# Performance work log

Hardware: AMD Instinct MI355X
Metric: run time of the kernel (lower is better)

The kernel has to match this reference:

```python
import jax, jax.numpy as jnp
import numpy as np

C = 128
B = 64
EPS = 1e-6


def _ln2d(x, w, b):
    # LayerNorm over channel dim (NAFNet-style LayerNorm2d), eps=1e-6
    mu = x.mean(axis=1, keepdims=True)
    var = ((x - mu) ** 2).mean(axis=1, keepdims=True)
    return (x - mu) / jnp.sqrt(var + EPS) * w[None, :, None, None] + b[None, :, None, None]


def _conv4(x, w, b):
    # Conv2d kernel 4, stride 4, no padding; NCHW / OIHW
    y = jax.lax.conv_general_dilated(x, w, (4, 4), 'VALID',
                                     dimension_numbers=('NCHW', 'OIHW', 'NCHW'))
    return y + b[None, :, None, None]


def _pixel_shuffle4(x):
    # (B, c*16, H, W) -> (B, c, 4H, 4W), torch PixelShuffle semantics
    b, c16, h, w = x.shape
    c = c16 // 16
    x = x.reshape(b, c, 4, 4, h, w)
    x = x.transpose(0, 1, 4, 2, 5, 3)
    return x.reshape(b, c, h * 4, w * 4)


def setup_inputs() -> dict:
    key = jax.random.key(0)
    ks = jax.random.split(key, 16)
    s = 0.02
    return {
        'x_l': jax.random.normal(ks[0], (B, C, 32, 32), jnp.float32),
        'x_r': jax.random.normal(ks[1], (B, C, 32, 32), jnp.float32),
        'ln_w_l': jnp.ones((C,), jnp.float32), 'ln_b_l': jnp.zeros((C,), jnp.float32),
        'ln_w_r': jnp.ones((C,), jnp.float32), 'ln_b_r': jnp.zeros((C,), jnp.float32),
        'Wl1': jax.random.normal(ks[2], (C, C, 4, 4), jnp.float32) * s,
        'bl1': jnp.zeros((C,), jnp.float32),
        'Wr1': jax.random.normal(ks[3], (C, C, 4, 4), jnp.float32) * s,
        'br1': jnp.zeros((C,), jnp.float32),
        'Wl2': jax.random.normal(ks[4], (C, C, 4, 4), jnp.float32) * s,
        'bl2': jnp.zeros((C,), jnp.float32),
        'Wr2': jax.random.normal(ks[5], (C, C, 4, 4), jnp.float32) * s,
        'br2': jnp.zeros((C,), jnp.float32),
        'pos': jax.random.normal(ks[6], (1, C, 8, 8), jnp.float32),
        'beta': jax.random.normal(ks[7], (1, C, 1, 1), jnp.float32) * s,
        'gamma': jax.random.normal(ks[8], (1, C, 1, 1), jnp.float32) * s,
        'Wl3': jax.random.normal(ks[9], (16 * C, C), jnp.float32) * s,
        'bl3': jnp.zeros((16 * C,), jnp.float32),
        'Wr3': jax.random.normal(ks[10], (16 * C, C), jnp.float32) * s,
        'br3': jnp.zeros((16 * C,), jnp.float32),
    }


def reference(x_l, x_r, ln_w_l, ln_b_l, ln_w_r, ln_b_r, Wl1, bl1, Wr1, br1,
              Wl2, bl2, Wr2, br2, pos, beta, gamma, Wl3, bl3, Wr3, br3):
    c = x_l.shape[1]
    scale = c ** (-0.5)
    B1 = x_l.shape[0]
    B2 = x_r.shape[0]

    Ql = _conv4(_ln2d(x_l, ln_w_l, ln_b_l), Wl1, bl1) + pos  # (B1,c,8,8)
    Qr = _conv4(_ln2d(x_r, ln_w_r, ln_b_r), Wr1, br1) + pos  # (B2,c,8,8)
    h1, w1 = Ql.shape[-2], Ql.shape[-1]
    h2, w2 = Qr.shape[-2], Qr.shape[-1]
    m1, m2 = h1 * w1, h2 * w2

    Qlm = Ql.transpose(0, 2, 3, 1).reshape(B1, m1, c)          # b (h w) c
    Qrm = Qr.transpose(1, 0, 2, 3).reshape(c, B2 * m2)         # c (b h w)
    Vl = (_conv4(x_l, Wl2, bl2) + pos).transpose(0, 2, 3, 1).reshape(B1 * m1, c)
    Vr = (_conv4(x_r, Wr2, br2) + pos).transpose(0, 2, 3, 1).reshape(B2 * m2, c)

    attn = jnp.matmul(Qlm, Qrm) * scale                        # (B1, m1, B2*m2)

    F_r2l = jnp.matmul(jax.nn.softmax(attn * (B2 ** (-0.5)), axis=-1), Vr)
    F_r2l = F_r2l.reshape(B1, h1, w1, c)

    attn2 = attn.reshape(B1, m1, B2, m2).transpose(2, 3, 0, 1).reshape(B2, m2, B1 * m1)
    F_l2r = jnp.matmul(jax.nn.softmax(attn2 * (B1 ** (-0.5)), axis=-1), Vl)
    F_l2r = F_l2r.reshape(B2, h2, w2, c)

    F_r2l = _pixel_shuffle4((jnp.matmul(F_r2l, Wl3.T) + bl3).transpose(0, 3, 1, 2)) * beta
    F_l2r = _pixel_shuffle4((jnp.matmul(F_l2r, Wr3.T) + br3).transpose(0, 3, 1, 2)) * gamma
    return (x_l + F_r2l, x_r + F_l2r)
```

## Files before the change

kernel.cpp:

```cpp
#include <hip/hip_runtime.h>
#include <stdint.h>

using bf16x8 = __attribute__((ext_vector_type(8))) short;
using f32x4  = __attribute__((ext_vector_type(4))) float;

__device__ __forceinline__ unsigned short f2bf(float f) {
  union { float f; uint32_t u; } v; v.f = f;
  uint32_t r = v.u + 0x7FFFu + ((v.u >> 16) & 1u);
  return (unsigned short)(r >> 16);
}
__device__ __forceinline__ uint32_t pk2(float a, float b) {
  return (uint32_t)f2bf(a) | ((uint32_t)f2bf(b) << 16);
}
__device__ __forceinline__ float bf2f(unsigned short s) {
  union { uint32_t u; float f; } v; v.u = ((uint32_t)s) << 16;
  return v.f;
}
__device__ __forceinline__ f32x4 mfma16(bf16x8 a, bf16x8 b, f32x4 c) {
  return __builtin_amdgcn_mfma_f32_16x16x32_bf16(a, b, c, 0, 0, 0);
}

__global__ __launch_bounds__(256) void k_prep(
    const float* __restrict__ xl, const float* __restrict__ xr,
    const float* __restrict__ lnwl, const float* __restrict__ lnbl,
    const float* __restrict__ lnwr, const float* __restrict__ lnbr,
    const float* __restrict__ Wl1, const float* __restrict__ bl1,
    const float* __restrict__ Wr1, const float* __restrict__ br1,
    const float* __restrict__ Wl2, const float* __restrict__ Wr2,
    const float* __restrict__ Wl3, const float* __restrict__ Wr3,
    float* __restrict__ muW, float* __restrict__ rsW,
    unsigned short* __restrict__ Wq, unsigned short* __restrict__ Wv,
    float* __restrict__ bqW, unsigned short* __restrict__ W3bf)
{
  const int gbid = blockIdx.x;
  const int t = threadIdx.x;
  __shared__ float red[4];

  if (gbid < 256) {
    const int bx = gbid;
    const int side = bx >> 7, rem = bx & 127;
    const int b = rem >> 1, half = rem & 1;
    const float* x = (side ? xr : xl) + (size_t)b * 131072 + half * 512;
    const int px = t * 2;
    float s0=0, s1=0, q0=0, q1=0;
#pragma unroll 4
    for (int c = 0; c < 128; ++c) {
      const float2 v = *(const float2*)(x + c*1024 + px);
      s0 += v.x; q0 += v.x*v.x;
      s1 += v.y; q1 += v.y*v.y;
    }
    const int o = (side*64 + b)*1024 + half*512 + px;
    float2 mu, rs;
    mu.x = s0*(1.0f/128.0f); mu.y = s1*(1.0f/128.0f);
    rs.x = rsqrtf(fmaxf(q0*(1.0f/128.0f) - mu.x*mu.x, 0.0f) + 1e-6f);
    rs.y = rsqrtf(fmaxf(q1*(1.0f/128.0f) - mu.y*mu.y, 0.0f) + 1e-6f);
    *(float2*)(muW + o) = mu;
    *(float2*)(rsW + o) = rs;
  } else if (gbid < 512) {
    const int bx = gbid - 256;
    const int side = bx >> 7, co = bx & 127;
    const float* W1  = side ? Wr1 : Wl1;
    const float* W2  = side ? Wr2 : Wl2;
    const float* b1  = side ? br1 : bl1;
    const float* lnw = side ? lnwr : lnwl;
    const float* lnb = side ? lnbr : lnbl;
    const int ci = t >> 1;
    const float lw = lnw[ci], lb = lnb[ci];

    const size_t dsto = (size_t)(side*32 + (t>>3))*8192 + (size_t)co*64 + (t&7)*8;

    const float* src1 = W1 + (size_t)co*2048 + t*8;
    const float4 a0 = *(const float4*)(src1);
    const float4 a1 = *(const float4*)(src1 + 4);
    float part = (a0.x+a0.y+a0.z+a0.w + a1.x+a1.y+a1.z+a1.w) * lb;
    uint4 pkq;
    pkq.x = pk2(a0.x*lw, a0.y*lw); pkq.y = pk2(a0.z*lw, a0.w*lw);
    pkq.z = pk2(a1.x*lw, a1.y*lw); pkq.w = pk2(a1.z*lw, a1.w*lw);
    *(uint4*)(Wq + dsto) = pkq;

    const float* src2 = W2 + (size_t)co*2048 + t*8;
    const float4 c0 = *(const float4*)(src2);
    const float4 c1 = *(const float4*)(src2 + 4);
    uint4 pkv;
    pkv.x = pk2(c0.x, c0.y); pkv.y = pk2(c0.z, c0.w);
    pkv.z = pk2(c1.x, c1.y); pkv.w = pk2(c1.z, c1.w);
    *(uint4*)(Wv + dsto) = pkv;

    float v = part;
    v += __shfl_down(v, 32, 64); v += __shfl_down(v, 16, 64);
    v += __shfl_down(v, 8, 64);  v += __shfl_down(v, 4, 64);
    v += __shfl_down(v, 2, 64);  v += __shfl_down(v, 1, 64);
    if ((t & 63) == 0) red[t >> 6] = v;
    __syncthreads();
    if (t == 0) bqW[side*128 + co] = b1[co] + red[0] + red[1] + red[2] + red[3];
  } else {
    const int b = gbid - 512;
    const float* src = (b < 256 ? Wl3 : Wr3) + (size_t)(b & 255) * 1024;
    const float4 v = *(const float4*)(src + t*4);
    *(uint2*)(W3bf + (size_t)b*1024 + t*4) = make_uint2(pk2(v.x, v.y), pk2(v.z, v.w));
  }
}

__global__ __launch_bounds__(256) void k_conv(
    const float* __restrict__ xl, const float* __restrict__ xr,
    const unsigned short* __restrict__ Wq, const unsigned short* __restrict__ Wv,
    const float* __restrict__ muW, const float* __restrict__ rsW,
    unsigned short* __restrict__ Cpart)
{
  const int bid = blockIdx.x;
  const int ks = bid & 3;
  const int img = (bid >> 2) & 63;
  const int ctype = bid >> 8;
  const int side = ctype & 1;
  const bool isQ = ctype < 2;
  const float* x = (side ? xr : xl) + (size_t)img * 131072;
  const unsigned short* Bsrc = (isQ ? Wq : Wv) + (size_t)side * 262144;

  const int t = threadIdx.x;
  const int w = t >> 6, l = t & 63, lo = l & 15, g = l >> 4;

  __shared__ __align__(16) unsigned char lds[24576];
  unsigned char* A = lds;
  unsigned char* B = lds + 8192;

  const int cl   = t >> 6;
  const int px0  = (t & 63) * 16;
  const int y    = px0 >> 5;
  const int wr   = y & 3;
  const int pbase = (y >> 2)*8 + ((px0 & 31) >> 2);

  float4 mu4[4], rs4[4];
  if (isQ) {
    const int o = (side*64 + img)*1024 + px0;
#pragma unroll
    for (int i = 0; i < 4; ++i) {
      mu4[i] = *(const float4*)(muW + o + 4*i);
      rs4[i] = *(const float4*)(rsW + o + 4*i);
    }
  }

  const int cout = t >> 1, part = t & 1;
  const int keyB = ((cout ^ (cout >> 3)) & 7) << 4;

  f32x4 acc[4][2];
#pragma unroll
  for (int a = 0; a < 4; ++a) { acc[a][0] = (f32x4)0.0f; acc[a][1] = (f32x4)0.0f; }

  for (int it = 0; it < 8; ++it) {
    const int kb = ks*8 + it;
    __syncthreads();
    {
      const float* xs = x + (size_t)(kb*4 + cl)*1024 + px0;
#pragma unroll
      for (int i = 0; i < 4; ++i) {
        float4 v = *(const float4*)(xs + 4*i);
        if (isQ) {
          v.x = (v.x - mu4[i].x)*rs4[i].x; v.y = (v.y - mu4[i].y)*rs4[i].y;
          v.z = (v.z - mu4[i].z)*rs4[i].z; v.w = (v.w - mu4[i].w)*rs4[i].w;
        }
        const int p = pbase + i;
        int dst = p*128 + cl*32 + wr*8;
        dst ^= ((p ^ (p >> 3)) & 7) << 4;
        *(uint2*)(A + dst) = make_uint2(pk2(v.x, v.y), pk2(v.z, v.w));
      }
    }
    {
      const unsigned short* bs = Bsrc + (size_t)kb*8192 + t*32;
#pragma unroll
      for (int i = 0; i < 4; ++i) {
        const bf16x8 v = *(const bf16x8*)(bs + i*8);
        *(bf16x8*)(B + cout*128 + ((part*64 + i*16) ^ keyB)) = v;
      }
    }
    __syncthreads();
    bf16x8 af[4][2], bfr[2][2];
#pragma unroll
    for (int mf = 0; mf < 4; ++mf) {
      const int row = mf*16 + lo;
      const int key = ((row ^ (row >> 3)) & 7) << 4;
#pragma unroll
      for (int kc = 0; kc < 2; ++kc)
        af[mf][kc] = *(const bf16x8*)(A + row*128 + ((kc*64 + g*16) ^ key));
    }
#pragma unroll
    for (int nf = 0; nf < 2; ++nf) {
      const int row = w*32 + nf*16 + lo;
      const int key = ((row ^ (row >> 3)) & 7) << 4;
#pragma unroll
      for (int kc = 0; kc < 2; ++kc)
        bfr[nf][kc] = *(const bf16x8*)(B + row*128 + ((kc*64 + g*16) ^ key));
    }
    __builtin_amdgcn_s_setprio(1);
#pragma unroll
    for (int kc = 0; kc < 2; ++kc)
#pragma unroll
      for (int nf = 0; nf < 2; ++nf)
#pragma unroll
        for (int mf = 0; mf < 4; ++mf)
          acc[mf][nf] = mfma16(af[mf][kc], bfr[nf][kc], acc[mf][nf]);
    __builtin_amdgcn_s_setprio(0);
  }

  unsigned short* Cp = Cpart + (size_t)bid * 8192;
#pragma unroll
  for (int mf = 0; mf < 4; ++mf)
#pragma unroll
    for (int nf = 0; nf < 2; ++nf) {
      const int c = w*32 + nf*16 + lo;
      const int p0 = mf*16 + g*4;
      *(uint2*)(Cp + c*64 + p0) =
          make_uint2(pk2(acc[mf][nf][0], acc[mf][nf][1]),
                     pk2(acc[mf][nf][2], acc[mf][nf][3]));
    }
}

__global__ __launch_bounds__(256) void k_convred(
    const unsigned short* __restrict__ Cpart,
    const float* __restrict__ bqW,
    const float* __restrict__ bl2, const float* __restrict__ br2,
    const float* __restrict__ pos,
    unsigned short* __restrict__ Qbf, unsigned short* __restrict__ Vtbf)
{
  const int bid2 = blockIdx.x;
  const int ctype = bid2 >> 6, img = bid2 & 63;
  const int side = ctype & 1;
  const bool isQ = ctype < 2;
  const int t = threadIdx.x;

  __shared__ float S[64][130];

  const int c = t >> 1, p0 = (t & 1) * 32;
  {
    float acc[32];
#pragma unroll
    for (int j = 0; j < 32; ++j) acc[j] = 0.f;
#pragma unroll
    for (int s = 0; s < 4; ++s) {
      const unsigned short* Cp = Cpart + ((size_t)(bid2*4 + s))*8192 + c*64 + p0;
#pragma unroll
      for (int j8 = 0; j8 < 4; ++j8) {
        const bf16x8 v = *(const bf16x8*)(Cp + j8*8);
#pragma unroll
        for (int e = 0; e < 8; ++e)
          acc[j8*8 + e] += bf2f((unsigned short)v[e]);
      }
    }
#pragma unroll
    for (int j = 0; j < 32; ++j) S[p0 + j][c] = acc[j];
  }
  __syncthreads();

  if (isQ) {
    const float* bq = bqW + side*128;
    const int p = t >> 2, c0 = (t & 3) * 32;
    const int rot = (t & 3) * 4;
    uint32_t pk[16];
#pragma unroll
    for (int j2 = 0; j2 < 16; ++j2) {
      const int jj = (j2 + rot) & 15;
      const int ca = c0 + jj*2;
      const float2 sv = *(const float2*)(&S[p][ca]);
      const float va = (sv.x + bq[ca]     + pos[ca*64 + p])     * 0.12625283f;
      const float vb = (sv.y + bq[ca + 1] + pos[(ca+1)*64 + p]) * 0.12625283f;
      pk[jj] = pk2(va, vb);
    }
    unsigned short* Qo = Qbf + (size_t)side*524288 + ((size_t)(img*64 + p))*128 + c0;
    *(uint4*)(Qo)      = make_uint4(pk[0],  pk[1],  pk[2],  pk[3]);
    *(uint4*)(Qo + 8)  = make_uint4(pk[4],  pk[5],  pk[6],  pk[7]);
    *(uint4*)(Qo + 16) = make_uint4(pk[8],  pk[9],  pk[10], pk[11]);
    *(uint4*)(Qo + 24) = make_uint4(pk[12], pk[13], pk[14], pk[15]);
  } else {
    const float* b2 = side ? br2 : bl2;
    const float bb = b2[c];
    uint32_t pk[16];
#pragma unroll
    for (int j2 = 0; j2 < 16; ++j2) {
      const int pa = p0 + j2*2;
      const float va = S[pa][c]     + bb + pos[c*64 + pa];
      const float vb = S[pa + 1][c] + bb + pos[c*64 + pa + 1];
      pk[j2] = pk2(va, vb);
    }
    unsigned short* Vo = Vtbf + (size_t)side*524288 + (size_t)c*4096 + img*64 + p0;
    *(uint4*)(Vo)      = make_uint4(pk[0],  pk[1],  pk[2],  pk[3]);
    *(uint4*)(Vo + 8)  = make_uint4(pk[4],  pk[5],  pk[6],  pk[7]);
    *(uint4*)(Vo + 16) = make_uint4(pk[8],  pk[9],  pk[10], pk[11]);
    *(uint4*)(Vo + 24) = make_uint4(pk[12], pk[13], pk[14], pk[15]);
  }
}

__global__ __launch_bounds__(256, 2) void k_attn(
    const unsigned short* __restrict__ Qbf,
    const unsigned short* __restrict__ Vtbf,
    float* __restrict__ Opart,
    float* __restrict__ Lpart)
{
  const int bid = blockIdx.x;
  const int xcd = bid & 7;
  const int dir = xcd >> 2;
  const int ks  = xcd & 3;
  const int qb  = bid >> 3;
  const unsigned short* Qp = Qbf  + (size_t)dir*524288;
  const unsigned short* Kp = Qbf  + (size_t)(1-dir)*524288;
  const unsigned short* Vp = Vtbf + (size_t)(1-dir)*524288;

  const int t = threadIdx.x;
  const int w = t >> 6, l = t & 63, lo = l & 15, g = l >> 4;

  __shared__ __align__(16) unsigned char lds[73728];
  unsigned char* ldsP = lds + 65536;
  __shared__ float lred[4][64];

  bf16x8 aq[4][4];
#pragma unroll
  for (int mf = 0; mf < 4; ++mf)
#pragma unroll
    for (int kc = 0; kc < 4; ++kc)
      aq[mf][kc] = *(const bf16x8*)(Qp + (size_t)(qb*64 + mf*16 + lo)*128 + kc*32 + g*8);

  f32x4 o[4][2];
#pragma unroll
  for (int a = 0; a < 4; ++a) { o[a][0] = (f32x4)0.0f; o[a][1] = (f32x4)0.0f; }
  float ls[4] = {0.f, 0.f, 0.f, 0.f};

  const int kt0 = ks * 16;

  const int ksrcBase = t ^ ((t >> 4) & 7);
  const int vc    = t >> 3;
  const int vi16  = (t & 7) * 16;
  const int vsoff = (vi16 ^ (((t >> 3) & 7) << 4)) >> 1;

  {
    const uint4* src = (const uint4*)(Kp + (size_t)kt0*8192);
#pragma unroll
    for (int j = 0; j < 4; ++j)
      *(uint4*)(lds + (t + 256*j)*16) = src[ksrcBase + 256*j];
#pragma unroll
    for (int j = 0; j < 4; ++j) {
      const int c = vc + 32*j;
      *(uint4*)(lds + 32768 + c*128 + vi16) =
          *(const uint4*)(Vp + (size_t)c*4096 + kt0*64 + vsoff);
    }
  }
  __syncthreads();

  for (int it = 0; it < 16; ++it) {
    const int cur = it & 1;
    unsigned char* curK = lds + cur*16384;
    unsigned char* curV = lds + 32768 + cur*16384;

    uint4 kr0, kr1, kr2, kr3, vr0, vr1, vr2, vr3;
    if (it < 15) {
      const int kt = kt0 + it + 1;
      const uint4* src = (const uint4*)(Kp + (size_t)kt*8192);
      kr0 = src[ksrcBase];
      kr1 = src[ksrcBase + 256];
      kr2 = src[ksrcBase + 512];
      kr3 = src[ksrcBase + 768];
      const unsigned short* vsrc = Vp + (size_t)kt*64 + vsoff;
      vr0 = *(const uint4*)(vsrc + (size_t)(vc     )*4096);
      vr1 = *(const uint4*)(vsrc + (size_t)(vc + 32)*4096);
      vr2 = *(const uint4*)(vsrc + (size_t)(vc + 64)*4096);
      vr3 = *(const uint4*)(vsrc + (size_t)(vc + 96)*4096);
    }

    f32x4 s[4];
    s[0] = (f32x4)0.0f; s[1] = (f32x4)0.0f; s[2] = (f32x4)0.0f; s[3] = (f32x4)0.0f;
    const int krow = w*16 + lo;
    const int keyk = (krow & 7) << 4;
    __builtin_amdgcn_s_setprio(1);
#pragma unroll
    for (int kc = 0; kc < 4; ++kc) {
      const bf16x8 bk = *(const bf16x8*)(curK + krow*256 + ((kc*64 + g*16) ^ keyk));
#pragma unroll
      for (int mf = 0; mf < 4; ++mf)
        s[mf] = mfma16(bk, aq[mf][kc], s[mf]);
    }
    __builtin_amdgcn_s_setprio(0);

#pragma unroll
    for (int mf = 0; mf < 4; ++mf) {
      const float e0 = exp2f(s[mf][0]);
      const float e1 = exp2f(s[mf][1]);
      const float e2 = exp2f(s[mf][2]);
      const float e3 = exp2f(s[mf][3]);
      ls[mf] += (e0 + e1) + (e2 + e3);
      const int q = mf*16 + lo;
      const int koff = (w*32 + g*8) ^ ((q & 7) << 4);
      *(uint2*)(ldsP + q*128 + koff) = make_uint2(pk2(e0, e1), pk2(e2, e3));
    }
    __syncthreads();

    __builtin_amdgcn_s_setprio(1);
#pragma unroll
    for (int kd = 0; kd < 2; ++kd) {
      bf16x8 pa[4];
#pragma unroll
      for (int mf = 0; mf < 4; ++mf) {
        const int q = mf*16 + lo;
        pa[mf] = *(const bf16x8*)(ldsP + q*128 + ((kd*64 + g*16) ^ ((q & 7) << 4)));
      }
#pragma unroll
      for (int nf = 0; nf < 2; ++nf) {
        const int c = w*32 + nf*16 + lo;
        const bf16x8 bv = *(const bf16x8*)(curV + c*128 + ((kd*64 + g*16) ^ ((c & 7) << 4)));
#pragma unroll
        for (int mf = 0; mf < 4; ++mf)
          o[mf][nf] = mfma16(pa[mf], bv, o[mf][nf]);
      }
    }
    __builtin_amdgcn_s_setprio(0);

    if (it < 15) {
      unsigned char* nK = lds + (cur ^ 1)*16384;
      unsigned char* nV = lds + 32768 + (cur ^ 1)*16384;
      *(uint4*)(nK + (t      )*16) = kr0;
      *(uint4*)(nK + (t + 256)*16) = kr1;
      *(uint4*)(nK + (t + 512)*16) = kr2;
      *(uint4*)(nK + (t + 768)*16) = kr3;
      *(uint4*)(nV + (vc     )*128 + vi16) = vr0;
      *(uint4*)(nV + (vc + 32)*128 + vi16) = vr1;
      *(uint4*)(nV + (vc + 64)*128 + vi16) = vr2;
      *(uint4*)(nV + (vc + 96)*128 + vi16) = vr3;
    }
    __syncthreads();
  }

#pragma unroll
  for (int mf = 0; mf < 4; ++mf) {
    float v = ls[mf];
    v += __shfl_xor(v, 16, 64);
    v += __shfl_xor(v, 32, 64);
    if (l < 16) lred[w][mf*16 + lo] = v;
  }
  __syncthreads();

  float* Ob = Opart + (((size_t)dir*64 + qb)*4 + ks)*64*128;
#pragma unroll
  for (int mf = 0; mf < 4; ++mf)
#pragma unroll
    for (int nf = 0; nf < 2; ++nf) {
      const int c = w*32 + nf*16 + lo;
#pragma unroll
      for (int rr = 0; rr < 4; ++rr) {
        const int q = mf*16 + g*4 + rr;
        Ob[q*128 + c] = o[mf][nf][rr];
      }
    }
  if (t < 64)
    Lpart[(((size_t)dir*64 + qb)*4 + ks)*64 + t] =
        lred[0][t] + lred[1][t] + lred[2][t] + lred[3][t];
}

__global__ __launch_bounds__(256) void k_reduce(
    const float* __restrict__ Opart, const float* __restrict__ Lpart,
    unsigned short* __restrict__ Fbf)
{
  const int bid = blockIdx.x;
  const int dir = bid >> 7, rb = bid & 127;
  const int t = threadIdx.x;
  const int qr = t >> 3;
  const int cs = (t & 7) * 16;
  const int r  = rb*32 + qr;
  const int qb = r >> 6, q = r & 63;
  const size_t pb = ((size_t)dir*64 + qb)*4;
  float acc[16];
#pragma unroll
  for (int i = 0; i < 16; ++i) acc[i] = 0.f;
  float lsum = 0.f;
#pragma unroll
  for (int s = 0; s < 4; ++s) {
    const float* Ob = Opart + ((pb + s)*64 + q)*128 + cs;
#pragma unroll
    for (int i = 0; i < 16; i += 4) {
      const float4 v = *(const float4*)(Ob + i);
      acc[i] += v.x; acc[i+1] += v.y; acc[i+2] += v.z; acc[i+3] += v.w;
    }
    lsum += Lpart[(pb + s)*64 + q];
  }
  const float inv = 1.0f / lsum;
  uint32_t pkw[8];
#pragma unroll
  for (int i = 0; i < 8; ++i) pkw[i] = pk2(acc[2*i]*inv, acc[2*i+1]*inv);
  unsigned short* Fo = Fbf + (size_t)dir*524288 + (size_t)r*128 + cs;
  *(uint4*)(Fo)     = make_uint4(pkw[0], pkw[1], pkw[2], pkw[3]);
  *(uint4*)(Fo + 8) = make_uint4(pkw[4], pkw[5], pkw[6], pkw[7]);
}

__global__ __launch_bounds__(256) void k_proj(
    const unsigned short* __restrict__ Fbf,
    const unsigned short* __restrict__ W3bf,
    const float* __restrict__ bl3, const float* __restrict__ br3,
    const float* __restrict__ beta, const float* __restrict__ gamma,
    const float* __restrict__ xl, const float* __restrict__ xr,
    float* __restrict__ out)
{
  const int nb = blockIdx.x, mb = blockIdx.y, side = blockIdx.z;
  const unsigned short* F  = Fbf + (size_t)side*524288 + (size_t)mb*8192;
  const unsigned short* W3 = W3bf + (size_t)side*262144 + (size_t)nb*16384;
  const float* b3  = (side ? br3 : bl3) + nb*128;
  const float* scl = side ? gamma : beta;
  const float* xin = (side ? xr : xl) + (size_t)mb*131072;
  float* op = out + (size_t)side*8388608 + (size_t)mb*131072;

  const int t = threadIdx.x;
  const int w = t >> 6, l = t & 63, lo = l & 15, g = l >> 4;

  __shared__ __align__(16) unsigned char lds[49152];
  unsigned char* Ft = lds;
  unsigned char* B3 = lds + 16384;
  float* Sf = (float*)lds;

  {
    const uint4* src = (const uint4*)F;
#pragma unroll
    for (int j = 0; j < 4; ++j) {
      const int idx = t + 256*j;
      const int dst = idx*16;
      const int row = dst >> 8;
      *(uint4*)(Ft + dst) = src[(dst ^ ((row & 7) << 4)) >> 4];
    }
  }
  {
    const int nl = t >> 1, half = t & 1;
    const unsigned short* wsrc = W3 + (size_t)nl*128 + half*64;
#pragma unroll
    for (int ch = 0; ch < 8; ++ch) {
      const uint4 v = *(const uint4*)(wsrc + ch*8);
      const int inrow = (half*128 + ch*16) ^ ((nl & 7) << 4);
      *(uint4*)(B3 + nl*256 + inrow) = v;
    }
  }
  __syncthreads();

  f32x4 acc[4][2];
#pragma unroll
  for (int a=0;a<4;a++) { acc[a][0] = (f32x4)0.0f; acc[a][1] = (f32x4)0.0f; }

  bf16x8 af[4][4];
#pragma unroll
  for (int mf = 0; mf < 4; ++mf) {
    const int row = mf*16 + lo;
#pragma unroll
    for (int kc = 0; kc < 4; ++kc)
      af[mf][kc] = *(const bf16x8*)(Ft + row*256 + ((kc*64 + g*16) ^ ((row & 7) << 4)));
  }
#pragma unroll
  for (int kc = 0; kc < 4; ++kc)
#pragma unroll
    for (int nf = 0; nf < 2; ++nf) {
      const int n = w*32 + nf*16 + lo;
      const bf16x8 bb = *(const bf16x8*)(B3 + n*256 + ((kc*64 + g*16) ^ ((n & 7) << 4)));
#pragma unroll
      for (int mf = 0; mf < 4; ++mf)
        acc[mf][nf] = mfma16(af[mf][kc], bb, acc[mf][nf]);
    }

  __syncthreads();

  {
    const int r4 = (lo >> 2) & 3, sc = lo & 3;
#pragma unroll
    for (int nf = 0; nf < 2; ++nf) {
      const int cl = w*2 + nf;
      const int n16 = w*32 + nf*16 + lo;
      const float scc = scl[nb*8 + cl];
      const float bb3 = b3[n16];
#pragma unroll
      for (int mf = 0; mf < 4; ++mf)
#pragma unroll
        for (int rr = 0; rr < 4; ++rr) {
          const int pi = mf*16 + g*4 + rr;
          const int h = pi >> 3, wc = pi & 7;
          Sf[cl*1032 + h*128 + r4*32 + wc*4 + sc] = scc*(acc[mf][nf][rr] + bb3);
        }
    }
  }
  __syncthreads();

#pragma unroll
  for (int j = 0; j < 8; ++j) {
    const int pix = t*4;
    const float4 s = *(const float4*)(Sf + j*1032 + pix);
    const size_t gaddr = (size_t)(nb*8 + j)*1024 + pix;
    const float4 xv = *(const float4*)(xin + gaddr);
    float4 r;
    r.x = xv.x + s.x; r.y = xv.y + s.y; r.z = xv.z + s.z; r.w = xv.w + s.w;
    *(float4*)(op + gaddr) = r;
  }
}

extern "C" void kernel_launch(void* const* d_in, const int* in_sizes, int n_in,
                              void* d_out, int out_size, void* d_ws, size_t ws_size,
                              hipStream_t stream) {
  (void)in_sizes; (void)n_in; (void)out_size; (void)ws_size;
  const float* xl   = (const float*)d_in[0];
  const float* xr   = (const float*)d_in[1];
  const float* lnwl = (const float*)d_in[2];
  const float* lnbl = (const float*)d_in[3];
  const float* lnwr = (const float*)d_in[4];
  const float* lnbr = (const float*)d_in[5];
  const float* Wl1  = (const float*)d_in[6];
  const float* bl1  = (const float*)d_in[7];
  const float* Wr1  = (const float*)d_in[8];
  const float* br1  = (const float*)d_in[9];
  const float* Wl2  = (const float*)d_in[10];
  const float* bl2  = (const float*)d_in[11];
  const float* Wr2  = (const float*)d_in[12];
  const float* br2  = (const float*)d_in[13];
  const float* pos  = (const float*)d_in[14];
  const float* beta = (const float*)d_in[15];
  const float* gamma= (const float*)d_in[16];
  const float* Wl3  = (const float*)d_in[17];
  const float* bl3  = (const float*)d_in[18];
  const float* Wr3  = (const float*)d_in[19];
  const float* br3  = (const float*)d_in[20];

  float* muW = (float*)d_ws;
  float* rsW = muW + 131072;
  float* bqW = rsW + 131072;
  unsigned short* Wq   = (unsigned short*)(bqW + 256);
  unsigned short* Wv   = Wq + 524288;
  unsigned short* Qbf  = Wv + 524288;
  unsigned short* Vtbf = Qbf + 1048576;
  unsigned short* Fbf  = Vtbf + 1048576;
  unsigned short* W3bf = Fbf + 1048576;
  unsigned short* Cpart = W3bf + 524288;
  float* Opart = (float*)Cpart;
  float* Lpart = (float*)(Cpart + 8388608);

  k_prep<<<1024, 256, 0, stream>>>(xl, xr, lnwl, lnbl, lnwr, lnbr,
      Wl1, bl1, Wr1, br1, Wl2, Wr2, Wl3, Wr3, muW, rsW, Wq, Wv, bqW, W3bf);
  k_conv<<<1024, 256, 0, stream>>>(xl, xr, Wq, Wv, muW, rsW, Cpart);
  k_convred<<<256, 256, 0, stream>>>(Cpart, bqW, bl2, br2, pos, Qbf, Vtbf);
  k_attn<<<512, 256, 0, stream>>>(Qbf, Vtbf, Opart, Lpart);
  k_reduce<<<256, 256, 0, stream>>>(Opart, Lpart, Fbf);
  k_proj<<<dim3(16, 64, 2), 256, 0, stream>>>(Fbf, W3bf, bl3, br3,
      beta, gamma, xl, xr, (float*)d_out);
}
```

Measured before the change: 123.1 us.

## Split attention key range eight ways with single-buffered LDS for higher occupancy

The attention kernel now splits the key dimension into 8 chunks instead of 4, which doubles the grid to 1024 blocks, and the reduce kernel sums 8 partials. LDS drops from double-buffered K/V (about 73 KB) to a single buffer (40 KB), and the launch bound is raised to 4 blocks per CU, aiming for more waves in flight and better latency hiding. The costs are an extra barrier per iteration, since the next tile's writes must wait for all reads, and twice as much partial O/L traffic written and then read by the reduce kernel. The block-to-XCD mapping also changes: all 8 splits of a query block now share one block-id group instead of being spread by XCD.

After: 176.4 us. 43.3% more time.

```diff
diff --git a/kernel.cpp b/kernel.cpp
--- a/kernel.cpp
+++ b/kernel.cpp
@@ -288,17 +288,16 @@
   }
 }
 
-__global__ __launch_bounds__(256, 2) void k_attn(
+__global__ __launch_bounds__(256, 4) void k_attn(
     const unsigned short* __restrict__ Qbf,
     const unsigned short* __restrict__ Vtbf,
     float* __restrict__ Opart,
     float* __restrict__ Lpart)
 {
   const int bid = blockIdx.x;
-  const int xcd = bid & 7;
-  const int dir = xcd >> 2;
-  const int ks  = xcd & 3;
-  const int qb  = bid >> 3;
+  const int ks  = bid & 7;
+  const int dir = (bid >> 3) & 1;
+  const int qb  = bid >> 4;
   const unsigned short* Qp = Qbf  + (size_t)dir*524288;
   const unsigned short* Kp = Qbf  + (size_t)(1-dir)*524288;
   const unsigned short* Vp = Vtbf + (size_t)(1-dir)*524288;
@@ -306,9 +305,11 @@
   const int t = threadIdx.x;
   const int w = t >> 6, l = t & 63, lo = l & 15, g = l >> 4;
 
-  __shared__ __align__(16) unsigned char lds[73728];
-  unsigned char* ldsP = lds + 65536;
-  __shared__ float lred[4][64];
+  __shared__ __align__(16) unsigned char lds[40960];
+  unsigned char* Kb = lds;
+  unsigned char* Vb = lds + 16384;
+  unsigned char* Pb = lds + 32768;
+  float* lred = (float*)lds;
 
   bf16x8 aq[4][4];
 #pragma unroll
@@ -322,7 +323,7 @@
   for (int a = 0; a < 4; ++a) { o[a][0] = (f32x4)0.0f; o[a][1] = (f32x4)0.0f; }
   float ls[4] = {0.f, 0.f, 0.f, 0.f};
 
-  const int kt0 = ks * 16;
+  const int kt0 = ks * 8;
 
   const int ksrcBase = t ^ ((t >> 4) & 7);
   const int vc    = t >> 3;
@@ -333,23 +334,19 @@
     const uint4* src = (const uint4*)(Kp + (size_t)kt0*8192);
 #pragma unroll
     for (int j = 0; j < 4; ++j)
-      *(uint4*)(lds + (t + 256*j)*16) = src[ksrcBase + 256*j];
+      *(uint4*)(Kb + (t + 256*j)*16) = src[ksrcBase + 256*j];
 #pragma unroll
     for (int j = 0; j < 4; ++j) {
       const int c = vc + 32*j;
-      *(uint4*)(lds + 32768 + c*128 + vi16) =
+      *(uint4*)(Vb + c*128 + vi16) =
           *(const uint4*)(Vp + (size_t)c*4096 + kt0*64 + vsoff);
     }
   }
   __syncthreads();
 
-  for (int it = 0; it < 16; ++it) {
-    const int cur = it & 1;
-    unsigned char* curK = lds + cur*16384;
-    unsigned char* curV = lds + 32768 + cur*16384;
-
+  for (int it = 0; it < 8; ++it) {
     uint4 kr0, kr1, kr2, kr3, vr0, vr1, vr2, vr3;
-    if (it < 15) {
+    if (it < 7) {
       const int kt = kt0 + it + 1;
       const uint4* src = (const uint4*)(Kp + (size_t)kt*8192);
       kr0 = src[ksrcBase];
@@ -370,7 +367,7 @@
     __builtin_amdgcn_s_setprio(1);
 #pragma unroll
     for (int kc = 0; kc < 4; ++kc) {
-      const bf16x8 bk = *(const bf16x8*)(curK + krow*256 + ((kc*64 + g*16) ^ keyk));
+      const bf16x8 bk = *(const bf16x8*)(Kb + krow*256 + ((kc*64 + g*16) ^ keyk));
 #pragma unroll
       for (int mf = 0; mf < 4; ++mf)
         s[mf] = mfma16(bk, aq[mf][kc], s[mf]);
@@ -386,7 +383,7 @@
       ls[mf] += (e0 + e1) + (e2 + e3);
       const int q = mf*16 + lo;
       const int koff = (w*32 + g*8) ^ ((q & 7) << 4);
-      *(uint2*)(ldsP + q*128 + koff) = make_uint2(pk2(e0, e1), pk2(e2, e3));
+      *(uint2*)(Pb + q*128 + koff) = make_uint2(pk2(e0, e1), pk2(e2, e3));
     }
     __syncthreads();
 
@@ -397,32 +394,31 @@
 #pragma unroll
       for (int mf = 0; mf < 4; ++mf) {
         const int q = mf*16 + lo;
-        pa[mf] = *(const bf16x8*)(ldsP + q*128 + ((kd*64 + g*16) ^ ((q & 7) << 4)));
+        pa[mf] = *(const bf16x8*)(Pb + q*128 + ((kd*64 + g*16) ^ ((q & 7) << 4)));
       }
 #pragma unroll
       for (int nf = 0; nf < 2; ++nf) {
         const int c = w*32 + nf*16 + lo;
-        const bf16x8 bv = *(const bf16x8*)(curV + c*128 + ((kd*64 + g*16) ^ ((c & 7) << 4)));
+        const bf16x8 bv = *(const bf16x8*)(Vb + c*128 + ((kd*64 + g*16) ^ ((c & 7) << 4)));
 #pragma unroll
         for (int mf = 0; mf < 4; ++mf)
           o[mf][nf] = mfma16(pa[mf], bv, o[mf][nf]);
       }
     }
     __builtin_amdgcn_s_setprio(0);
-
-    if (it < 15) {
-      unsigned char* nK = lds + (cur ^ 1)*16384;
-      unsigned char* nV = lds + 32768 + (cur ^ 1)*16384;
-      *(uint4*)(nK + (t      )*16) = kr0;
-      *(uint4*)(nK + (t + 256)*16) = kr1;
-      *(uint4*)(nK + (t + 512)*16) = kr2;
-      *(uint4*)(nK + (t + 768)*16) = kr3;
-      *(uint4*)(nV + (vc     )*128 + vi16) = vr0;
-      *(uint4*)(nV + (vc + 32)*128 + vi16) = vr1;
-      *(uint4*)(nV + (vc + 64)*128 + vi16) = vr2;
-      *(uint4*)(nV + (vc + 96)*128 + vi16) = vr3;
-    }
     __syncthreads();
+
+    if (it < 7) {
+      *(uint4*)(Kb + (t      )*16) = kr0;
+      *(uint4*)(Kb + (t + 256)*16) = kr1;
+      *(uint4*)(Kb + (t + 512)*16) = kr2;
+      *(uint4*)(Kb + (t + 768)*16) = kr3;
+      *(uint4*)(Vb + (vc     )*128 + vi16) = vr0;
+      *(uint4*)(Vb + (vc + 32)*128 + vi16) = vr1;
+      *(uint4*)(Vb + (vc + 64)*128 + vi16) = vr2;
+      *(uint4*)(Vb + (vc + 96)*128 + vi16) = vr3;
+      __syncthreads();
+    }
   }
 
 #pragma unroll
@@ -430,11 +426,11 @@
     float v = ls[mf];
     v += __shfl_xor(v, 16, 64);
     v += __shfl_xor(v, 32, 64);
-    if (l < 16) lred[w][mf*16 + lo] = v;
+    if (l < 16) lred[w*64 + mf*16 + lo] = v;
   }
   __syncthreads();
 
-  float* Ob = Opart + (((size_t)dir*64 + qb)*4 + ks)*64*128;
+  float* Ob = Opart + (((size_t)dir*64 + qb)*8 + ks)*64*128;
 #pragma unroll
   for (int mf = 0; mf < 4; ++mf)
 #pragma unroll
@@ -447,8 +443,8 @@
       }
     }
   if (t < 64)
-    Lpart[(((size_t)dir*64 + qb)*4 + ks)*64 + t] =
-        lred[0][t] + lred[1][t] + lred[2][t] + lred[3][t];
+    Lpart[(((size_t)dir*64 + qb)*8 + ks)*64 + t] =
+        lred[t] + lred[64 + t] + lred[128 + t] + lred[192 + t];
 }
 
 __global__ __launch_bounds__(256) void k_reduce(
@@ -462,13 +458,13 @@
   const int cs = (t & 7) * 16;
   const int r  = rb*32 + qr;
   const int qb = r >> 6, q = r & 63;
-  const size_t pb = ((size_t)dir*64 + qb)*4;
+  const size_t pb = ((size_t)dir*64 + qb)*8;
   float acc[16];
 #pragma unroll
   for (int i = 0; i < 16; ++i) acc[i] = 0.f;
   float lsum = 0.f;
 #pragma unroll
-  for (int s = 0; s < 4; ++s) {
+  for (int s = 0; s < 8; ++s) {
     const float* Ob = Opart + ((pb + s)*64 + q)*128 + cs;
 #pragma unroll
     for (int i = 0; i < 16; i += 4) {
@@ -626,13 +622,13 @@
   unsigned short* W3bf = Fbf + 1048576;
   unsigned short* Cpart = W3bf + 524288;
   float* Opart = (float*)Cpart;
-  float* Lpart = (float*)(Cpart + 8388608);
+  float* Lpart = Opart + 8388608;
 
   k_prep<<<1024, 256, 0, stream>>>(xl, xr, lnwl, lnbl, lnwr, lnbr,
       Wl1, bl1, Wr1, br1, Wl2, Wr2, Wl3, Wr3, muW, rsW, Wq, Wv, bqW, W3bf);
   k_conv<<<1024, 256, 0, stream>>>(xl, xr, Wq, Wv, muW, rsW, Cpart);
   k_convred<<<256, 256, 0, stream>>>(Cpart, bqW, bl2, br2, pos, Qbf, Vtbf);
-  k_attn<<<512, 256, 0, stream>>>(Qbf, Vtbf, Opart, Lpart);
+  k_attn<<<1024, 256, 0, stream>>>(Qbf, Vtbf, Opart, Lpart);
   k_reduce<<<256, 256, 0, stream>>>(Opart, Lpart, Fbf);
   k_proj<<<dim3(16, 64, 2), 256, 0, stream>>>(Fbf, W3bf, bl3, br3,
       beta, gamma, xl, xr, (float*)d_out);
```

## Load V fragments directly from global into registers, shrink LDS for occupancy

Applied to the files above, without the earlier changes.

The attention kernel stops staging the transposed V tiles through double-buffered shared memory. Each wave now loads its own V MFMA operand fragments straight from global memory at the start of every iteration. This cuts the LDS footprint from about 72KB to 40KB, and launch bounds are raised to 3 blocks per CU to use the freed space. The trade-off is that V loads are no longer prefetched one iteration ahead, so global latency may be exposed unless the added occupancy hides it. Some V data may also be read redundantly across waves.

After: 142.5 us. 15.7% more time.

```diff
diff --git a/kernel.cpp b/kernel.cpp
--- a/kernel.cpp
+++ b/kernel.cpp
@@ -288,7 +288,7 @@
   }
 }
 
-__global__ __launch_bounds__(256, 2) void k_attn(
+__global__ __launch_bounds__(256, 3) void k_attn(
     const unsigned short* __restrict__ Qbf,
     const unsigned short* __restrict__ Vtbf,
     float* __restrict__ Opart,
@@ -306,8 +306,8 @@
   const int t = threadIdx.x;
   const int w = t >> 6, l = t & 63, lo = l & 15, g = l >> 4;
 
-  __shared__ __align__(16) unsigned char lds[73728];
-  unsigned char* ldsP = lds + 65536;
+  __shared__ __align__(16) unsigned char lds[40960];
+  unsigned char* ldsP = lds + 32768;
   __shared__ float lred[4][64];
 
   bf16x8 aq[4][4];
@@ -323,44 +323,37 @@
   float ls[4] = {0.f, 0.f, 0.f, 0.f};
 
   const int kt0 = ks * 16;
-
   const int ksrcBase = t ^ ((t >> 4) & 7);
-  const int vc    = t >> 3;
-  const int vi16  = (t & 7) * 16;
-  const int vsoff = (vi16 ^ (((t >> 3) & 7) << 4)) >> 1;
+
+  const unsigned short* vrow0 = Vp + (size_t)(w*32 + lo)*4096 + g*8 + (size_t)kt0*64;
+  const unsigned short* vrow1 = vrow0 + (size_t)16*4096;
 
   {
     const uint4* src = (const uint4*)(Kp + (size_t)kt0*8192);
 #pragma unroll
     for (int j = 0; j < 4; ++j)
       *(uint4*)(lds + (t + 256*j)*16) = src[ksrcBase + 256*j];
-#pragma unroll
-    for (int j = 0; j < 4; ++j) {
-      const int c = vc + 32*j;
-      *(uint4*)(lds + 32768 + c*128 + vi16) =
-          *(const uint4*)(Vp + (size_t)c*4096 + kt0*64 + vsoff);
-    }
   }
   __syncthreads();
 
   for (int it = 0; it < 16; ++it) {
     const int cur = it & 1;
     unsigned char* curK = lds + cur*16384;
-    unsigned char* curV = lds + 32768 + cur*16384;
-
-    uint4 kr0, kr1, kr2, kr3, vr0, vr1, vr2, vr3;
+
+    const unsigned short* vt0 = vrow0 + it*64;
+    const unsigned short* vt1 = vrow1 + it*64;
+    const bf16x8 vf00 = *(const bf16x8*)(vt0);
+    const bf16x8 vf01 = *(const bf16x8*)(vt0 + 32);
+    const bf16x8 vf10 = *(const bf16x8*)(vt1);
+    const bf16x8 vf11 = *(const bf16x8*)(vt1 + 32);
+
+    uint4 kr0, kr1, kr2, kr3;
     if (it < 15) {
-      const int kt = kt0 + it + 1;
-      const uint4* src = (const uint4*)(Kp + (size_t)kt*8192);
+      const uint4* src = (const uint4*)(Kp + (size_t)(kt0 + it + 1)*8192);
       kr0 = src[ksrcBase];
       kr1 = src[ksrcBase + 256];
       kr2 = src[ksrcBase + 512];
       kr3 = src[ksrcBase + 768];
-      const unsigned short* vsrc = Vp + (size_t)kt*64 + vsoff;
-      vr0 = *(const uint4*)(vsrc + (size_t)(vc     )*4096);
-      vr1 = *(const uint4*)(vsrc + (size_t)(vc + 32)*4096);
-      vr2 = *(const uint4*)(vsrc + (size_t)(vc + 64)*4096);
-      vr3 = *(const uint4*)(vsrc + (size_t)(vc + 96)*4096);
     }
 
     f32x4 s[4];
@@ -391,36 +384,34 @@
     __syncthreads();
 
     __builtin_amdgcn_s_setprio(1);
-#pragma unroll
-    for (int kd = 0; kd < 2; ++kd) {
-      bf16x8 pa[4];
+    {
+      bf16x8 pa0[4], pa1[4];
 #pragma unroll
       for (int mf = 0; mf < 4; ++mf) {
         const int q = mf*16 + lo;
-        pa[mf] = *(const bf16x8*)(ldsP + q*128 + ((kd*64 + g*16) ^ ((q & 7) << 4)));
+        const int key = (q & 7) << 4;
+        pa0[mf] = *(const bf16x8*)(ldsP + q*128 + ((g*16      ) ^ key));
+        pa1[mf] = *(const bf16x8*)(ldsP + q*128 + ((64 + g*16 ) ^ key));
       }
 #pragma unroll
-      for (int nf = 0; nf < 2; ++nf) {
-        const int c = w*32 + nf*16 + lo;
-        const bf16x8 bv = *(const bf16x8*)(curV + c*128 + ((kd*64 + g*16) ^ ((c & 7) << 4)));
-#pragma unroll
-        for (int mf = 0; mf < 4; ++mf)
-          o[mf][nf] = mfma16(pa[mf], bv, o[mf][nf]);
+      for (int mf = 0; mf < 4; ++mf) {
+        o[mf][0] = mfma16(pa0[mf], vf00, o[mf][0]);
+        o[mf][1] = mfma16(pa0[mf], vf10, o[mf][1]);
+      }
+#pragma unroll
+      for (int mf = 0; mf < 4; ++mf) {
+        o[mf][0] = mfma16(pa1[mf], vf01, o[mf][0]);
+        o[mf][1] = mfma16(pa1[mf], vf11, o[mf][1]);
       }
     }
     __builtin_amdgcn_s_setprio(0);
 
     if (it < 15) {
       unsigned char* nK = lds + (cur ^ 1)*16384;
-      unsigned char* nV = lds + 32768 + (cur ^ 1)*16384;
       *(uint4*)(nK + (t      )*16) = kr0;
       *(uint4*)(nK + (t + 256)*16) = kr1;
       *(uint4*)(nK + (t + 512)*16) = kr2;
       *(uint4*)(nK + (t + 768)*16) = kr3;
-      *(uint4*)(nV + (vc     )*128 + vi16) = vr0;
-      *(uint4*)(nV + (vc + 32)*128 + vi16) = vr1;
-      *(uint4*)(nV + (vc + 64)*128 + vi16) = vr2;
-      *(uint4*)(nV + (vc + 96)*128 + vi16) = vr3;
     }
     __syncthreads();
   }
```
